# Optimization experiments

Measured on AMD Instinct MI355X. Metric: run time of the kernel, lower is better.

Reference implementation:

```python
import jax, jax.numpy as jnp
import numpy as np
from jax import lax

B, C, A = 32, 84, 8400      # batch, 4+nc channels, anchors (640x640, strides 8/16/32)
NC = 80                     # num classes
K = 1000                    # max_det
CONF_THRES = 0.1
IOU_THRES = 0.7
MAX_WH = 7680.0             # class offset for non-agnostic NMS (ultralytics constant)
SCALE = min(640.0 / 1080.0, 640.0 / 1920.0)  # letterbox scale (input 640, orig 1920x1080)


def setup_inputs() -> dict:
    key = jax.random.key(0)
    k1, k2, k3 = jax.random.split(key, 3)
    # YOLOv8 head output: rows 0:4 are decoded xywh boxes in input pixels, rows 4: are sigmoided class scores
    cxcy = jax.random.uniform(k1, (B, 2, A), jnp.float32, 0.0, 640.0)
    wh = jax.random.uniform(k2, (B, 2, A), jnp.float32, 8.0, 120.0)
    scores = jax.random.uniform(k3, (B, NC, A), jnp.float32, 0.0, 1.0)
    preds = jnp.concatenate([cxcy, wh, scores], axis=1)  # [B, 84, A]
    return {"preds": preds}


def _xywh2xyxy(b):
    cx, cy, w, h = b[:, 0], b[:, 1], b[:, 2], b[:, 3]
    return jnp.stack([cx - w / 2, cy - h / 2, cx + w / 2, cy + h / 2], axis=1)


def _pairwise_iou(b):  # b: [K,4] xyxy
    area = (b[:, 2] - b[:, 0]) * (b[:, 3] - b[:, 1])
    lt = jnp.maximum(b[:, None, :2], b[None, :, :2])
    rb = jnp.minimum(b[:, None, 2:], b[None, :, 2:])
    wh = jnp.clip(rb - lt, 0.0)
    inter = wh[..., 0] * wh[..., 1]
    return inter / (area[:, None] + area[None, :] - inter + 1e-7)


def _nms_per_image(p):  # p: [84, A]
    boxes = _xywh2xyxy(p[:4].T)          # [A,4]
    cls_scores = p[4:]                   # [NC, A]
    conf = jnp.max(cls_scores, axis=0)   # best-class confidence (multi_label=False)
    cls = jnp.argmax(cls_scores, axis=0).astype(jnp.float32)
    # conf threshold + class filter (classes=[0])
    valid = (conf > CONF_THRES) & (cls == 0.0)
    masked = jnp.where(valid, conf, -1.0)
    top_s, idx = lax.top_k(masked, K)    # candidates sorted by score desc
    top_boxes = boxes[idx]               # [K,4]
    top_cls = cls[idx]
    top_valid = top_s > CONF_THRES
    # class-offset boxes for non-agnostic NMS (agnostic=False)
    nms_boxes = top_boxes + top_cls[:, None] * MAX_WH
    iou = _pairwise_iou(nms_boxes)       # [K,K]
    ar = jnp.arange(K)

    def body(i, keep):
        suppress = (iou[i] > IOU_THRES) & keep[i] & (ar > i)
        return keep & ~suppress

    keep = lax.fori_loop(0, K, body, top_valid)
    out_boxes = top_boxes / SCALE        # rescale to original image coords
    out = jnp.concatenate(
        [out_boxes, top_s[:, None], top_cls[:, None]], axis=1)  # [K,6]
    return jnp.where(keep[:, None], out, 0.0)


def reference(preds):
    # [B, K, 6]: x1,y1,x2,y2 (original-image coords), score, class
    return jax.vmap(_nms_per_image)(preds)
```

## Files before the change

### kernel.cpp

```cpp
#include <hip/hip_runtime.h>

#define BATCH 32
#define CH    84
#define NA    8400
#define KTOP  1000
#define MAXC  512
#define GROUPS 2100
#define SLICES 33
#define IOU_T 0.7f

__global__ __launch_bounds__(256) void cand_kernel(const float* __restrict__ preds,
        int* __restrict__ counts, float* __restrict__ cscore, int* __restrict__ cidx) {
    int b = blockIdx.x / SLICES;
    int slice = blockIdx.x - b * SLICES;
    int t = threadIdx.x;
    int gl = t >> 2, chunk = t & 3;
    int g = slice * 64 + gl;
    bool active = g < GROUPS;

    __shared__ int lcount, lbase;
    __shared__ float lsc[256];
    __shared__ int   lix[256];
    if (t == 0) lcount = 0;
    __syncthreads();

    const float* base = preds + (size_t)b * (CH * NA);
    float mx = -1.f, my = -1.f, mz = -1.f, mw = -1.f;
    if (active) {
        int c0 = 5 + chunk * 20;
        int c1 = (chunk == 3) ? CH : c0 + 20;
        const float* p = base + (size_t)c0 * NA + 4 * g;
        for (int c = c0; c < c1; ++c, p += NA) {
            float4 v = *(const float4*)p;
            mx = fmaxf(mx, v.x); my = fmaxf(my, v.y);
            mz = fmaxf(mz, v.z); mw = fmaxf(mw, v.w);
        }
    }
    mx = fmaxf(mx, __shfl_xor(mx, 1)); my = fmaxf(my, __shfl_xor(my, 1));
    mz = fmaxf(mz, __shfl_xor(mz, 1)); mw = fmaxf(mw, __shfl_xor(mw, 1));
    mx = fmaxf(mx, __shfl_xor(mx, 2)); my = fmaxf(my, __shfl_xor(my, 2));
    mz = fmaxf(mz, __shfl_xor(mz, 2)); mw = fmaxf(mw, __shfl_xor(mw, 2));

    if (active && chunk == 0) {
        float4 s0 = *(const float4*)(base + (size_t)4 * NA + 4 * g);
        float s[4] = {s0.x, s0.y, s0.z, s0.w};
        float m[4] = {mx, my, mz, mw};
        #pragma unroll
        for (int k = 0; k < 4; ++k) {
            if (s[k] > 0.1f && s[k] >= m[k]) {
                int p_ = atomicAdd(&lcount, 1);
                lsc[p_] = s[k];
                lix[p_] = 4 * g + k;
            }
        }
    }
    __syncthreads();
    if (t == 0) lbase = atomicAdd(&counts[b], lcount);
    __syncthreads();
    int nloc = lcount, bs = lbase;
    for (int i = t; i < nloc; i += 256) {
        int p_ = bs + i;
        if (p_ < MAXC) {
            cscore[b * MAXC + p_] = lsc[i];
            cidx[b * MAXC + p_]   = lix[i];
        }
    }
}

template<int S>
__device__ unsigned int nms_scan(int n, int lane, const float4* bxy, const float* ars) {
    float ox1[S], oy1[S], ox2[S], oy2[S], oar[S];
    unsigned int keep = 0u;
    #pragma unroll
    for (int k = 0; k < S; ++k) {
        int c = k * 64 + lane;
        if (c < n) {
            float4 v = bxy[c];
            ox1[k] = v.x; oy1[k] = v.y; ox2[k] = v.z; oy2[k] = v.w;
            oar[k] = ars[c];
            keep |= (1u << k);
        } else {
            ox1[k] = 0.f; oy1[k] = 0.f; ox2[k] = -1.f; oy2[k] = -1.f; oar[k] = 0.f;
        }
    }
    for (int i = 0; i < n; ++i) {
        int which = i >> 6, src = i & 63;
        int mybit = (keep >> which) & 1;
        unsigned long long bal = __ballot(mybit);
        if ((bal >> src) & 1ull) {
            float4 bi = bxy[i];
            float ai = ars[i];
            #pragma unroll
            for (int k = 0; k < S; ++k) {
                float lx = fmaxf(bi.x, ox1[k]), ly = fmaxf(bi.y, oy1[k]);
                float rx = fminf(bi.z, ox2[k]), ry = fminf(bi.w, oy2[k]);
                float iw = fmaxf(rx - lx, 0.0f), ih = fmaxf(ry - ly, 0.0f);
                float inter = iw * ih;
                float iou = inter / (ai + oar[k] - inter + 1e-7f);
                int c = k * 64 + lane;
                if (c > i && iou > IOU_T) keep &= ~(1u << k);
            }
        }
    }
    return keep;
}

__global__ __launch_bounds__(256) void nms_kernel(const float* __restrict__ preds,
        const int* __restrict__ counts, const float* __restrict__ cscore,
        const int* __restrict__ cidx, float* __restrict__ out) {
    int b = blockIdx.x;
    int tid = threadIdx.x;

    __shared__ float rs[MAXC]; __shared__ int ri[MAXC];
    __shared__ float ss[MAXC]; __shared__ int sa[MAXC];
    __shared__ float4 bxy[MAXC];
    __shared__ float  ars[MAXC];
    __shared__ unsigned int keepm[64];

    int n = counts[b];
    if (n > MAXC) n = MAXC;

    for (int i = tid; i < n; i += 256) { rs[i] = cscore[b * MAXC + i]; ri[i] = cidx[b * MAXC + i]; }
    __syncthreads();

    for (int i = tid; i < n; i += 256) {
        float si = rs[i]; int ii = ri[i];
        int r = 0;
        for (int j = 0; j < n; ++j) {
            float sj = rs[j]; int ij = ri[j];
            if (sj > si || (sj == si && ij < ii)) r++;
        }
        ss[r] = si; sa[r] = ii;
    }
    __syncthreads();

    const float* base = preds + (size_t)b * (CH * NA);
    for (int i = tid; i < n; i += 256) {
        int a = sa[i];
        float cx = base[a], cy = base[NA + a];
        float w  = base[2 * NA + a], h = base[3 * NA + a];
        float hx = w * 0.5f, hy = h * 0.5f;
        float X1 = cx - hx, Y1 = cy - hy, X2 = cx + hx, Y2 = cy + hy;
        bxy[i] = make_float4(X1, Y1, X2, Y2);
        ars[i] = (X2 - X1) * (Y2 - Y1);
    }
    __syncthreads();

    if (tid < 64) {
        unsigned int kp;
        if (n <= 128)      kp = nms_scan<2>(n, tid, bxy, ars);
        else if (n <= 256) kp = nms_scan<4>(n, tid, bxy, ars);
        else               kp = nms_scan<8>(n, tid, bxy, ars);
        keepm[tid] = kp;
    }
    __syncthreads();

    float* ob = out + (size_t)b * KTOP * 6;
    const float SCALEF = (float)(640.0 / 1920.0);
    for (int r = tid; r < KTOP; r += 256) {
        float v0 = 0.f, v1 = 0.f, v2 = 0.f, v3 = 0.f, v4 = 0.f, v5 = 0.f;
        if (r < n && ((keepm[r & 63] >> (r >> 6)) & 1u)) {
            float4 bx = bxy[r];
            v0 = bx.x / SCALEF; v1 = bx.y / SCALEF;
            v2 = bx.z / SCALEF; v3 = bx.w / SCALEF;
            v4 = ss[r]; v5 = 0.0f;
        }
        ob[r * 6 + 0] = v0; ob[r * 6 + 1] = v1; ob[r * 6 + 2] = v2;
        ob[r * 6 + 3] = v3; ob[r * 6 + 4] = v4; ob[r * 6 + 5] = v5;
    }
}

extern "C" void kernel_launch(void* const* d_in, const int* in_sizes, int n_in,
                              void* d_out, int out_size, void* d_ws, size_t ws_size,
                              hipStream_t stream) {
    const float* preds = (const float*)d_in[0];
    float* out = (float*)d_out;

    int*   counts = (int*)d_ws;
    float* cscore = (float*)((char*)d_ws + 128);
    int*   cidx   = (int*)((char*)d_ws + 128 + (size_t)BATCH * MAXC * sizeof(float));

    hipMemsetAsync(d_ws, 0, 128, stream);
    cand_kernel<<<BATCH * SLICES, 256, 0, stream>>>(preds, counts, cscore, cidx);
    nms_kernel<<<BATCH, 256, 0, stream>>>(preds, counts, cscore, cidx, out);
}
```

Before: 172.3 us.

## Use fixed per-slice candidate slots instead of global atomic compaction and memset

Each candidate block writes its survivors into a fixed per-slice slot and records its own count, so the global atomicAdd, the second block barrier and the workspace memset are no longer needed. The NMS kernel prefix-sums the 33 slice counts and compacts the candidates into shared memory. The class-max loop now has a fixed trip count of 20 with partial unrolling. Each slice keeps at most 32 candidates, which could drop candidates in dense slices. The larger candidate buffer also adds an nms_scan<17> path that raises register pressure.

Result: faster. 168.2 us (-2.4%).

```diff
diff --git a/kernel.cpp b/kernel.cpp
--- a/kernel.cpp
+++ b/kernel.cpp
@@ -4,9 +4,10 @@
 #define CH    84
 #define NA    8400
 #define KTOP  1000
-#define MAXC  512
 #define GROUPS 2100
 #define SLICES 33
+#define SLOT   32
+#define MAXC   (SLICES*SLOT)
 #define IOU_T 0.7f
 
 __global__ __launch_bounds__(256) void cand_kernel(const float* __restrict__ preds,
@@ -18,7 +19,7 @@
     int g = slice * 64 + gl;
     bool active = g < GROUPS;
 
-    __shared__ int lcount, lbase;
+    __shared__ int lcount;
     __shared__ float lsc[256];
     __shared__ int   lix[256];
     if (t == 0) lcount = 0;
@@ -27,10 +28,10 @@
     const float* base = preds + (size_t)b * (CH * NA);
     float mx = -1.f, my = -1.f, mz = -1.f, mw = -1.f;
     if (active) {
-        int c0 = 5 + chunk * 20;
-        int c1 = (chunk == 3) ? CH : c0 + 20;
+        int c0 = (chunk < 3) ? (5 + 20 * chunk) : 64;
         const float* p = base + (size_t)c0 * NA + 4 * g;
-        for (int c = c0; c < c1; ++c, p += NA) {
+        #pragma unroll 5
+        for (int k = 0; k < 20; ++k, p += NA) {
             float4 v = *(const float4*)p;
             mx = fmaxf(mx, v.x); my = fmaxf(my, v.y);
             mz = fmaxf(mz, v.z); mw = fmaxf(mw, v.w);
@@ -55,15 +56,11 @@
         }
     }
     __syncthreads();
-    if (t == 0) lbase = atomicAdd(&counts[b], lcount);
-    __syncthreads();
-    int nloc = lcount, bs = lbase;
-    for (int i = t; i < nloc; i += 256) {
-        int p_ = bs + i;
-        if (p_ < MAXC) {
-            cscore[b * MAXC + p_] = lsc[i];
-            cidx[b * MAXC + p_]   = lix[i];
-        }
+    int n = lcount; if (n > SLOT) n = SLOT;
+    if (t == 0) counts[b * SLICES + slice] = n;
+    if (t < n) {
+        cscore[b * MAXC + slice * SLOT + t] = lsc[t];
+        cidx[b * MAXC + slice * SLOT + t]   = lix[t];
     }
 }
 
@@ -111,16 +108,32 @@
     int b = blockIdx.x;
     int tid = threadIdx.x;
 
+    __shared__ int scnt[SLICES], soff[SLICES + 1];
     __shared__ float rs[MAXC]; __shared__ int ri[MAXC];
     __shared__ float ss[MAXC]; __shared__ int sa[MAXC];
     __shared__ float4 bxy[MAXC];
     __shared__ float  ars[MAXC];
     __shared__ unsigned int keepm[64];
 
-    int n = counts[b];
-    if (n > MAXC) n = MAXC;
+    if (tid < SLICES) scnt[tid] = counts[b * SLICES + tid];
+    __syncthreads();
+    if (tid == 0) {
+        int acc = 0;
+        #pragma unroll
+        for (int s_ = 0; s_ < SLICES; ++s_) { soff[s_] = acc; acc += scnt[s_]; }
+        soff[SLICES] = acc;
+    }
+    __syncthreads();
+    int n = soff[SLICES];
 
-    for (int i = tid; i < n; i += 256) { rs[i] = cscore[b * MAXC + i]; ri[i] = cidx[b * MAXC + i]; }
+    for (int t = tid; t < SLICES * SLOT; t += 256) {
+        int slice = t >> 5, j = t & (SLOT - 1);
+        if (j < scnt[slice]) {
+            int dst = soff[slice] + j;
+            rs[dst] = cscore[b * MAXC + t];
+            ri[dst] = cidx[b * MAXC + t];
+        }
+    }
     __syncthreads();
 
     for (int i = tid; i < n; i += 256) {
@@ -150,7 +163,8 @@
         unsigned int kp;
         if (n <= 128)      kp = nms_scan<2>(n, tid, bxy, ars);
         else if (n <= 256) kp = nms_scan<4>(n, tid, bxy, ars);
-        else               kp = nms_scan<8>(n, tid, bxy, ars);
+        else if (n <= 512) kp = nms_scan<8>(n, tid, bxy, ars);
+        else               kp = nms_scan<17>(n, tid, bxy, ars);
         keepm[tid] = kp;
     }
     __syncthreads();
@@ -177,10 +191,9 @@
     float* out = (float*)d_out;
 
     int*   counts = (int*)d_ws;
-    float* cscore = (float*)((char*)d_ws + 128);
-    int*   cidx   = (int*)((char*)d_ws + 128 + (size_t)BATCH * MAXC * sizeof(float));
+    float* cscore = (float*)((char*)d_ws + 16384);
+    int*   cidx   = (int*)((char*)d_ws + 16384 + (size_t)BATCH * MAXC * sizeof(float));
 
-    hipMemsetAsync(d_ws, 0, 128, stream);
     cand_kernel<<<BATCH * SLICES, 256, 0, stream>>>(preds, counts, cscore, cidx);
     nms_kernel<<<BATCH, 256, 0, stream>>>(preds, counts, cscore, cidx, out);
 }
```
